# Kernel optimization log

Hardware: AMD Instinct MI355X
Metric: run time of the kernel (lower is better)

## Reference

```python
import jax, jax.numpy as jnp
import numpy as np

EMBED = 512
HEADS = 8
HEAD_LEN = EMBED // HEADS  # 64


def setup_inputs() -> dict:
    key = jax.random.key(0)
    ks = jax.random.split(key, 8)
    B, L = 8, 2048
    return {
        "query": jax.random.normal(ks[0], (B, L, EMBED), dtype=jnp.float32),
        "key": jax.random.normal(ks[1], (B, L, EMBED), dtype=jnp.float32),
        "value": jax.random.normal(ks[2], (B, L, EMBED), dtype=jnp.float32),
        "Wq": jax.random.normal(ks[3], (HEAD_LEN, HEAD_LEN), dtype=jnp.float32) * 0.05,
        "Wk": jax.random.normal(ks[4], (HEAD_LEN, HEAD_LEN), dtype=jnp.float32) * 0.05,
        "Wv": jax.random.normal(ks[5], (HEAD_LEN, HEAD_LEN), dtype=jnp.float32) * 0.05,
        "Wo": jax.random.normal(ks[6], (EMBED, EMBED), dtype=jnp.float32) * 0.05,
        "bo": jax.random.normal(ks[7], (EMBED,), dtype=jnp.float32) * 0.05,
    }


def reference(query, key, value, Wq, Wk, Wv, Wo, bo):
    B, Lq, E = query.shape
    Lk = key.shape[1]
    Lv = value.shape[1]
    H, d = HEADS, HEAD_LEN
    # Faithful to original: q/k reshaped to (B, H, L, d) (splits the sequence
    # dim, not the feature dim); v reshaped to (B, L, H, d).
    q = query.reshape(B, H, Lq, d) @ Wq.T   # nn.Linear: x @ W^T
    k = key.reshape(B, H, Lk, d) @ Wk.T
    v = value.reshape(B, Lv, H, d) @ Wv.T
    scores = jnp.einsum('bhqf,bhkf->bhqk', q, k) / (E ** 0.5)  # scale = sqrt(embed_size)
    w = jax.nn.softmax(scores, axis=3)
    out = jnp.einsum('bhql,blhd->bqhd', w, v).reshape(B, Lq, H * d)
    return out @ Wo.T + bo
```

## Files before the change

kernel.cpp:

```cpp
#include <hip/hip_runtime.h>
#include <stdint.h>

#define BB 8
#define LL 2048
#define EE 512
#define HH 8
#define DD 64

typedef __attribute__((ext_vector_type(8))) short short8;
typedef __attribute__((ext_vector_type(4))) float f32x4;

#define QSCALE 0.06376435773361453f

__device__ __forceinline__ uint32_t pk2bf(float a, float b) {
    union { float f; uint32_t u; } va, vb; va.f = a; vb.f = b;
    return __builtin_amdgcn_perm(vb.u + 0x8000u, va.u + 0x8000u, 0x07060302u);
}

__device__ __forceinline__ short8 pack8(const float4 t0, const float4 t1) {
    union { uint32_t u[4]; short8 s; } r;
    r.u[0] = pk2bf(t0.x, t0.y); r.u[1] = pk2bf(t0.z, t0.w);
    r.u[2] = pk2bf(t1.x, t1.y); r.u[3] = pk2bf(t1.z, t1.w);
    return r.s;
}

__global__ __launch_bounds__(256) void prep_weights(const float* __restrict__ Wq, const float* __restrict__ Wk,
                                                    const float* __restrict__ Wv, const float* __restrict__ Wo,
                                                    short* __restrict__ WqB, short* __restrict__ WkB,
                                                    short* __restrict__ WvB, short* __restrict__ WoB) {
    int i = blockIdx.x * 256 + threadIdx.x;
    const float* src; short* dst; int off;
    if (i < 1024)      { src = Wq; dst = WqB; off = i; }
    else if (i < 2048) { src = Wk; dst = WkB; off = i - 1024; }
    else if (i < 3072) { src = Wv; dst = WvB; off = i - 2048; }
    else               { src = Wo; dst = WoB; off = i - 3072; }
    float4 t = reinterpret_cast<const float4*>(src)[off];
    uint2 d; d.x = pk2bf(t.x, t.y); d.y = pk2bf(t.z, t.w);
    reinterpret_cast<uint2*>(dst)[off] = d;
}

__global__ __launch_bounds__(256) void proj_fused(const float* __restrict__ query, const float* __restrict__ key,
                                                  const float* __restrict__ value,
                                                  const short* __restrict__ WqB, const short* __restrict__ WkB,
                                                  const short* __restrict__ WvB,
                                                  short* __restrict__ Oq, short* __restrict__ Ok, short* __restrict__ OvT) {
    const int id = blockIdx.x;
    const int lane = threadIdx.x & 63;
    const int wave = threadIdx.x >> 6;
    const int quad = lane >> 4;
    const int c    = lane & 15;

    if (id < 4096) {
        const bool isq = id < 2048;
        const float* X = isq ? query : key;
        const short* W = isq ? WqB : WkB;
        short* O = isq ? Oq : Ok;
        const float oscale = isq ? QSCALE : 1.0f;
        const int xid = isq ? id : id - 2048;
        const long r0 = (long)xid * 64 + wave * 16;

        short8 xb[2];
#pragma unroll
        for (int kk = 0; kk < 2; ++kk) {
            const float* src = X + (r0 + c) * 64 + kk * 32 + quad * 8;
            xb[kk] = pack8(*reinterpret_cast<const float4*>(src), *reinterpret_cast<const float4*>(src + 4));
        }

        f32x4 acc[4];
#pragma unroll
        for (int ft = 0; ft < 4; ++ft) { acc[ft][0]=0.f; acc[ft][1]=0.f; acc[ft][2]=0.f; acc[ft][3]=0.f; }

#pragma unroll
        for (int ft = 0; ft < 4; ++ft)
#pragma unroll
            for (int kk = 0; kk < 2; ++kk) {
                short8 wa = *reinterpret_cast<const short8*>(W + (ft * 16 + c) * 64 + kk * 32 + quad * 8);
                acc[ft] = __builtin_amdgcn_mfma_f32_16x16x32_bf16(wa, xb[kk], acc[ft], 0, 0, 0);
            }

#pragma unroll
        for (int ft = 0; ft < 4; ++ft) {
            uint2 d;
            d.x = pk2bf(acc[ft][0] * oscale, acc[ft][1] * oscale);
            d.y = pk2bf(acc[ft][2] * oscale, acc[ft][3] * oscale);
            *reinterpret_cast<uint2*>(O + (r0 + c) * 64 + ft * 16 + quad * 4) = d;
        }
    } else {
        const int vid = id - 4096;
        const int bh = vid >> 5, lt = vid & 31;
        const int b = bh >> 3, h = bh & 7;
        const int l0 = lt * 64 + wave * 16;

        short8 xa[2];
#pragma unroll
        for (int kk = 0; kk < 2; ++kk) {
            const float* src = value + ((long)(b * LL + l0 + c) * EE + h * 64) + kk * 32 + quad * 8;
            xa[kk] = pack8(*reinterpret_cast<const float4*>(src), *reinterpret_cast<const float4*>(src + 4));
        }

        f32x4 acc[4];
#pragma unroll
        for (int nt = 0; nt < 4; ++nt) { acc[nt][0]=0.f; acc[nt][1]=0.f; acc[nt][2]=0.f; acc[nt][3]=0.f; }

#pragma unroll
        for (int nt = 0; nt < 4; ++nt)
#pragma unroll
            for (int kk = 0; kk < 2; ++kk) {
                short8 wb = *reinterpret_cast<const short8*>(WvB + (nt * 16 + c) * 64 + kk * 32 + quad * 8);
                acc[nt] = __builtin_amdgcn_mfma_f32_16x16x32_bf16(xa[kk], wb, acc[nt], 0, 0, 0);
            }

#pragma unroll
        for (int nt = 0; nt < 4; ++nt) {
            uint2 d;
            d.x = pk2bf(acc[nt][0], acc[nt][1]);
            d.y = pk2bf(acc[nt][2], acc[nt][3]);
            *reinterpret_cast<uint2*>(OvT + ((long)bh * 64 + nt * 16 + c) * LL + l0 + quad * 4) = d;
        }
    }
}

#define PSTR 72

__global__ __launch_bounds__(256, 2) void attn_kernel(const short* __restrict__ Q, const short* __restrict__ K,
                                                      const short* __restrict__ VT, short* __restrict__ Oattn) {
    __shared__ __align__(16) short p_lds[2][4][64 * PSTR];
    const int lane = threadIdx.x & 63;
    const int wave = threadIdx.x >> 6;
    const int quad = lane >> 4;
    const int c    = lane & 15;
    const int bh = blockIdx.x & 63;
    const int qs = blockIdx.x >> 6;
    const int b = bh >> 3, h = bh & 7;
    const int q0 = qs * 256 + wave * 64;

    short8 aq[4][2];
#pragma unroll
    for (int t = 0; t < 4; ++t)
#pragma unroll
        for (int hh = 0; hh < 2; ++hh)
            aq[t][hh] = *reinterpret_cast<const short8*>(Q + ((long)bh * LL + q0 + t * 16 + c) * 64 + hh * 32 + quad * 8);

    f32x4 of[4][4];
#pragma unroll
    for (int t = 0; t < 4; ++t)
#pragma unroll
        for (int ft = 0; ft < 4; ++ft) { of[t][ft][0]=0.f; of[t][ft][1]=0.f; of[t][ft][2]=0.f; of[t][ft][3]=0.f; }
    float l[4] = {0.f, 0.f, 0.f, 0.f};

    const short* Kbase = K  + (long)bh * LL * 64;
    const short* Vbase = VT + (long)bh * 64 * LL;

#pragma unroll 2
    for (int kt = 0; kt < 32; ++kt) {
        const int kb = kt * 64;
        short* sl = p_lds[kt & 1][wave];

        short8 kf[4][2], vf[4][2];
#pragma unroll
        for (int nt = 0; nt < 4; ++nt) {
            const short* kp = Kbase + (long)(kb + nt * 16 + c) * 64 + quad * 8;
            kf[nt][0] = *reinterpret_cast<const short8*>(kp);
            kf[nt][1] = *reinterpret_cast<const short8*>(kp + 32);
            const short* vp = Vbase + (long)(nt * 16 + c) * LL + kb + quad * 8;
            vf[nt][0] = *reinterpret_cast<const short8*>(vp);
            vf[nt][1] = *reinterpret_cast<const short8*>(vp + 32);
        }

#pragma unroll
        for (int t = 0; t < 4; ++t) {
            f32x4 s[4];
#pragma unroll
            for (int nt = 0; nt < 4; ++nt) {
                f32x4 z; z[0]=0.f; z[1]=0.f; z[2]=0.f; z[3]=0.f;
                z = __builtin_amdgcn_mfma_f32_16x16x32_bf16(kf[nt][0], aq[t][0], z, 0, 0, 0);
                s[nt] = __builtin_amdgcn_mfma_f32_16x16x32_bf16(kf[nt][1], aq[t][1], z, 0, 0, 0);
            }
#pragma unroll
            for (int nt = 0; nt < 4; ++nt) {
                const float p0 = __builtin_amdgcn_exp2f(s[nt][0]), p1 = __builtin_amdgcn_exp2f(s[nt][1]);
                const float p2 = __builtin_amdgcn_exp2f(s[nt][2]), p3 = __builtin_amdgcn_exp2f(s[nt][3]);
                l[t] += (p0 + p1) + (p2 + p3);
                uint2 d; d.x = pk2bf(p0, p1); d.y = pk2bf(p2, p3);
                *reinterpret_cast<uint2*>(sl + (t * 16 + c) * PSTR + nt * 16 + quad * 4) = d;
            }
        }

#pragma unroll
        for (int t = 0; t < 4; ++t) {
            short8 ap0 = *reinterpret_cast<const short8*>(sl + (t * 16 + c) * PSTR + quad * 8);
            short8 ap1 = *reinterpret_cast<const short8*>(sl + (t * 16 + c) * PSTR + 32 + quad * 8);
#pragma unroll
            for (int ft = 0; ft < 4; ++ft) {
                of[t][ft] = __builtin_amdgcn_mfma_f32_16x16x32_bf16(vf[ft][0], ap0, of[t][ft], 0, 0, 0);
                of[t][ft] = __builtin_amdgcn_mfma_f32_16x16x32_bf16(vf[ft][1], ap1, of[t][ft], 0, 0, 0);
            }
        }
    }

    float inv[4];
#pragma unroll
    for (int t = 0; t < 4; ++t) {
        l[t] += __shfl_xor(l[t], 16);
        l[t] += __shfl_xor(l[t], 32);
        inv[t] = 1.0f / l[t];
    }

#pragma unroll
    for (int t = 0; t < 4; ++t) {
        const long row = (long)b * LL + q0 + t * 16 + c;
#pragma unroll
        for (int ft = 0; ft < 4; ++ft) {
            const float v0 = of[t][ft][0] * inv[t], v1 = of[t][ft][1] * inv[t];
            const float v2 = of[t][ft][2] * inv[t], v3 = of[t][ft][3] * inv[t];
            uint2 d; d.x = pk2bf(v0, v1); d.y = pk2bf(v2, v3);
            *reinterpret_cast<uint2*>(Oattn + row * EE + h * 64 + ft * 16 + quad * 4) = d;
        }
    }
}

__global__ __launch_bounds__(256) void out_proj(const short* __restrict__ A, const short* __restrict__ WoB,
                                                const float* __restrict__ bo, float* __restrict__ out) {
    const int lane = threadIdx.x & 63;
    const int wave = threadIdx.x >> 6;
    const int quad = lane >> 4;
    const int c    = lane & 15;
    const int nb = blockIdx.x;
    const int rb = blockIdx.y;
    const long r0 = (long)rb * 64 + wave * 16;

    f32x4 acc[4];
#pragma unroll
    for (int ft = 0; ft < 4; ++ft) { acc[ft][0]=0.f; acc[ft][1]=0.f; acc[ft][2]=0.f; acc[ft][3]=0.f; }

    for (int ks = 0; ks < 16; ++ks) {
        short8 bfr = *reinterpret_cast<const short8*>(A + (r0 + c) * EE + ks * 32 + quad * 8);
#pragma unroll
        for (int ft = 0; ft < 4; ++ft) {
            short8 afr = *reinterpret_cast<const short8*>(WoB + ((long)(nb * 64 + ft * 16 + c)) * EE + ks * 32 + quad * 8);
            acc[ft] = __builtin_amdgcn_mfma_f32_16x16x32_bf16(afr, bfr, acc[ft], 0, 0, 0);
        }
    }

#pragma unroll
    for (int ft = 0; ft < 4; ++ft) {
        float4 bias = *reinterpret_cast<const float4*>(bo + nb * 64 + ft * 16 + quad * 4);
        float4 res;
        res.x = acc[ft][0] + bias.x; res.y = acc[ft][1] + bias.y;
        res.z = acc[ft][2] + bias.z; res.w = acc[ft][3] + bias.w;
        *reinterpret_cast<float4*>(out + (r0 + c) * EE + nb * 64 + ft * 16 + quad * 4) = res;
    }
}

extern "C" void kernel_launch(void* const* d_in, const int* in_sizes, int n_in,
                              void* d_out, int out_size, void* d_ws, size_t ws_size,
                              hipStream_t stream) {
    const float* query = (const float*)d_in[0];
    const float* key   = (const float*)d_in[1];
    const float* value = (const float*)d_in[2];
    const float* Wq    = (const float*)d_in[3];
    const float* Wk    = (const float*)d_in[4];
    const float* Wv    = (const float*)d_in[5];
    const float* Wo    = (const float*)d_in[6];
    const float* bo    = (const float*)d_in[7];
    float* out = (float*)d_out;

    char* ws = (char*)d_ws;
    const size_t SZ = 16777216;
    short* q_ws    = (short*)(ws);
    short* k_ws    = (short*)(ws + SZ);
    short* vT_ws   = (short*)(ws + 2 * SZ);
    short* attn_ws = (short*)(ws + 3 * SZ);
    short* wo_ws   = (short*)(ws + 4 * SZ);
    short* wq_ws   = (short*)(ws + 4 * SZ + 524288);
    short* wk_ws   = (short*)(ws + 4 * SZ + 532480);
    short* wv_ws   = (short*)(ws + 4 * SZ + 540672);

    prep_weights<<<268, 256, 0, stream>>>(Wq, Wk, Wv, Wo, wq_ws, wk_ws, wv_ws, wo_ws);
    proj_fused<<<6144, 256, 0, stream>>>(query, key, value, wq_ws, wk_ws, wv_ws, q_ws, k_ws, vT_ws);
    attn_kernel<<<512, 256, 0, stream>>>(q_ws, k_ws, vT_ws, attn_ws);
    out_proj<<<dim3(8, 256), 256, 0, stream>>>(attn_ws, wo_ws, bo, out);
}
```

Baseline: 363.5 us.

## Switch attention to 32x32x16 MFMA and pass P through registers via permlane32 swap

```diff
diff --git a/kernel.cpp b/kernel.cpp
--- a/kernel.cpp
+++ b/kernel.cpp
@@ -9,6 +9,8 @@
 
 typedef __attribute__((ext_vector_type(8))) short short8;
 typedef __attribute__((ext_vector_type(4))) float f32x4;
+typedef __attribute__((ext_vector_type(16))) float f32x16;
+typedef __attribute__((ext_vector_type(2))) unsigned int u32x2v;
 
 #define QSCALE 0.06376435773361453f
 
@@ -120,102 +122,106 @@
     }
 }
 
-#define PSTR 72
-
 __global__ __launch_bounds__(256, 2) void attn_kernel(const short* __restrict__ Q, const short* __restrict__ K,
                                                       const short* __restrict__ VT, short* __restrict__ Oattn) {
-    __shared__ __align__(16) short p_lds[2][4][64 * PSTR];
     const int lane = threadIdx.x & 63;
     const int wave = threadIdx.x >> 6;
-    const int quad = lane >> 4;
-    const int c    = lane & 15;
+    const int hl = lane >> 5;
+    const int c  = lane & 31;
     const int bh = blockIdx.x & 63;
     const int qs = blockIdx.x >> 6;
-    const int b = bh >> 3, h = bh & 7;
+    const int b = bh >> 3, head = bh & 7;
     const int q0 = qs * 256 + wave * 64;
 
-    short8 aq[4][2];
-#pragma unroll
-    for (int t = 0; t < 4; ++t)
-#pragma unroll
-        for (int hh = 0; hh < 2; ++hh)
-            aq[t][hh] = *reinterpret_cast<const short8*>(Q + ((long)bh * LL + q0 + t * 16 + c) * 64 + hh * 32 + quad * 8);
-
-    f32x4 of[4][4];
-#pragma unroll
-    for (int t = 0; t < 4; ++t)
-#pragma unroll
-        for (int ft = 0; ft < 4; ++ft) { of[t][ft][0]=0.f; of[t][ft][1]=0.f; of[t][ft][2]=0.f; of[t][ft][3]=0.f; }
-    float l[4] = {0.f, 0.f, 0.f, 0.f};
-
-    const short* Kbase = K  + (long)bh * LL * 64;
-    const short* Vbase = VT + (long)bh * 64 * LL;
-
-#pragma unroll 2
-    for (int kt = 0; kt < 32; ++kt) {
-        const int kb = kt * 64;
-        short* sl = p_lds[kt & 1][wave];
-
-        short8 kf[4][2], vf[4][2];
-#pragma unroll
-        for (int nt = 0; nt < 4; ++nt) {
-            const short* kp = Kbase + (long)(kb + nt * 16 + c) * 64 + quad * 8;
-            kf[nt][0] = *reinterpret_cast<const short8*>(kp);
-            kf[nt][1] = *reinterpret_cast<const short8*>(kp + 32);
-            const short* vp = Vbase + (long)(nt * 16 + c) * LL + kb + quad * 8;
-            vf[nt][0] = *reinterpret_cast<const short8*>(vp);
-            vf[nt][1] = *reinterpret_cast<const short8*>(vp + 32);
-        }
-
-#pragma unroll
-        for (int t = 0; t < 4; ++t) {
-            f32x4 s[4];
-#pragma unroll
-            for (int nt = 0; nt < 4; ++nt) {
-                f32x4 z; z[0]=0.f; z[1]=0.f; z[2]=0.f; z[3]=0.f;
-                z = __builtin_amdgcn_mfma_f32_16x16x32_bf16(kf[nt][0], aq[t][0], z, 0, 0, 0);
-                s[nt] = __builtin_amdgcn_mfma_f32_16x16x32_bf16(kf[nt][1], aq[t][1], z, 0, 0, 0);
-            }
-#pragma unroll
-            for (int nt = 0; nt < 4; ++nt) {
-                const float p0 = __builtin_amdgcn_exp2f(s[nt][0]), p1 = __builtin_amdgcn_exp2f(s[nt][1]);
-                const float p2 = __builtin_amdgcn_exp2f(s[nt][2]), p3 = __builtin_amdgcn_exp2f(s[nt][3]);
-                l[t] += (p0 + p1) + (p2 + p3);
-                uint2 d; d.x = pk2bf(p0, p1); d.y = pk2bf(p2, p3);
-                *reinterpret_cast<uint2*>(sl + (t * 16 + c) * PSTR + nt * 16 + quad * 4) = d;
-            }
-        }
-
-#pragma unroll
-        for (int t = 0; t < 4; ++t) {
-            short8 ap0 = *reinterpret_cast<const short8*>(sl + (t * 16 + c) * PSTR + quad * 8);
-            short8 ap1 = *reinterpret_cast<const short8*>(sl + (t * 16 + c) * PSTR + 32 + quad * 8);
-#pragma unroll
-            for (int ft = 0; ft < 4; ++ft) {
-                of[t][ft] = __builtin_amdgcn_mfma_f32_16x16x32_bf16(vf[ft][0], ap0, of[t][ft], 0, 0, 0);
-                of[t][ft] = __builtin_amdgcn_mfma_f32_16x16x32_bf16(vf[ft][1], ap1, of[t][ft], 0, 0, 0);
-            }
-        }
-    }
-
-    float inv[4];
-#pragma unroll
-    for (int t = 0; t < 4; ++t) {
-        l[t] += __shfl_xor(l[t], 16);
+    short8 aq[2][4];
+#pragma unroll
+    for (int t = 0; t < 2; ++t)
+#pragma unroll
+        for (int ks = 0; ks < 4; ++ks)
+            aq[t][ks] = *reinterpret_cast<const short8*>(Q + ((long)bh * LL + q0 + t * 32 + c) * 64 + ks * 16 + hl * 8);
+
+    f32x16 of[2][2];
+#pragma unroll
+    for (int t = 0; t < 2; ++t)
+#pragma unroll
+        for (int ft = 0; ft < 2; ++ft)
+#pragma unroll
+            for (int i = 0; i < 16; ++i) of[t][ft][i] = 0.f;
+    float l[2] = {0.f, 0.f};
+
+    const short* Kb = K  + (long)bh * LL * 64;
+    const short* Vb = VT + (long)bh * 64 * LL;
+
+    for (int kb = 0; kb < LL; kb += 64) {
+        short8 kf[2][4], vf[2][4];
+#pragma unroll
+        for (int kt = 0; kt < 2; ++kt)
+#pragma unroll
+            for (int ks = 0; ks < 4; ++ks)
+                kf[kt][ks] = *reinterpret_cast<const short8*>(Kb + (long)(kb + kt * 32 + c) * 64 + ks * 16 + hl * 8);
+#pragma unroll
+        for (int ft = 0; ft < 2; ++ft)
+#pragma unroll
+            for (int kk = 0; kk < 4; ++kk)
+                vf[ft][kk] = *reinterpret_cast<const short8*>(Vb + (long)(ft * 32 + c) * LL + kb + kk * 16 + hl * 8);
+
+#pragma unroll
+        for (int t = 0; t < 2; ++t)
+#pragma unroll
+            for (int kt = 0; kt < 2; ++kt) {
+                f32x16 s;
+#pragma unroll
+                for (int i = 0; i < 16; ++i) s[i] = 0.f;
+#pragma unroll
+                for (int ks = 0; ks < 4; ++ks)
+                    s = __builtin_amdgcn_mfma_f32_32x32x16_bf16(kf[kt][ks], aq[t][ks], s, 0, 0, 0);
+
+                uint32_t xd[4][2];
+                float lac = 0.f;
+#pragma unroll
+                for (int g = 0; g < 4; ++g) {
+                    const float p0 = __builtin_amdgcn_exp2f(s[4 * g + 0]);
+                    const float p1 = __builtin_amdgcn_exp2f(s[4 * g + 1]);
+                    const float p2 = __builtin_amdgcn_exp2f(s[4 * g + 2]);
+                    const float p3 = __builtin_amdgcn_exp2f(s[4 * g + 3]);
+                    lac += (p0 + p1) + (p2 + p3);
+                    xd[g][0] = pk2bf(p0, p1);
+                    xd[g][1] = pk2bf(p2, p3);
+                }
+                l[t] += lac;
+
+#pragma unroll
+                for (int kt2 = 0; kt2 < 2; ++kt2) {
+                    u32x2v rA = __builtin_amdgcn_permlane32_swap(xd[2 * kt2][0], xd[2 * kt2 + 1][0], false, false);
+                    u32x2v rB = __builtin_amdgcn_permlane32_swap(xd[2 * kt2][1], xd[2 * kt2 + 1][1], false, false);
+                    union { uint32_t u[4]; short8 s8; } pb;
+                    pb.u[0] = rA[0]; pb.u[1] = rB[0]; pb.u[2] = rA[1]; pb.u[3] = rB[1];
+                    const int kk = kt * 2 + kt2;
+                    of[t][0] = __builtin_amdgcn_mfma_f32_32x32x16_bf16(vf[0][kk], pb.s8, of[t][0], 0, 0, 0);
+                    of[t][1] = __builtin_amdgcn_mfma_f32_32x32x16_bf16(vf[1][kk], pb.s8, of[t][1], 0, 0, 0);
+                }
+            }
+    }
+
+    float inv[2];
+#pragma unroll
+    for (int t = 0; t < 2; ++t) {
         l[t] += __shfl_xor(l[t], 32);
         inv[t] = 1.0f / l[t];
     }
 
 #pragma unroll
-    for (int t = 0; t < 4; ++t) {
-        const long row = (long)b * LL + q0 + t * 16 + c;
-#pragma unroll
-        for (int ft = 0; ft < 4; ++ft) {
-            const float v0 = of[t][ft][0] * inv[t], v1 = of[t][ft][1] * inv[t];
-            const float v2 = of[t][ft][2] * inv[t], v3 = of[t][ft][3] * inv[t];
-            uint2 d; d.x = pk2bf(v0, v1); d.y = pk2bf(v2, v3);
-            *reinterpret_cast<uint2*>(Oattn + row * EE + h * 64 + ft * 16 + quad * 4) = d;
-        }
+    for (int t = 0; t < 2; ++t) {
+        const long row = (long)b * LL + q0 + t * 32 + c;
+#pragma unroll
+        for (int ft = 0; ft < 2; ++ft)
+#pragma unroll
+            for (int g = 0; g < 4; ++g) {
+                const float v0 = of[t][ft][4 * g + 0] * inv[t], v1 = of[t][ft][4 * g + 1] * inv[t];
+                const float v2 = of[t][ft][4 * g + 2] * inv[t], v3 = of[t][ft][4 * g + 3] * inv[t];
+                uint2 d; d.x = pk2bf(v0, v1); d.y = pk2bf(v2, v3);
+                *reinterpret_cast<uint2*>(Oattn + row * EE + head * 64 + ft * 32 + g * 8 + hl * 4) = d;
+            }
     }
 }
 
```

After: 360.0 us. No clear change (-0.9%).
